# Kernel tuning notes

Hardware: AMD Instinct MI355X
Metric: run time of the kernel (lower is better)

## Reference

```python
import jax, jax.numpy as jnp
import numpy as np

H = W = 32
CROP = int(H * 0.8)  # 25, matches int(H*crop_ratio) in torch
MEAN = jnp.array([0.5071, 0.4867, 0.4408], jnp.float32).reshape(1, 3, 1, 1)
STD = jnp.array([0.2675, 0.2565, 0.2761], jnp.float32).reshape(1, 3, 1, 1)


def _bilinear(img, iy, ix):
    # img [C,H,W]; iy/ix [H,W] float pixel coords (reflected+clamped already)
    y0 = jnp.floor(iy); x0 = jnp.floor(ix)
    wy = iy - y0; wx = ix - x0
    y0i = jnp.clip(y0.astype(jnp.int32), 0, H - 1); y1i = jnp.clip(y0i + 1, 0, H - 1)
    x0i = jnp.clip(x0.astype(jnp.int32), 0, W - 1); x1i = jnp.clip(x0i + 1, 0, W - 1)
    v00 = img[:, y0i, x0i]; v01 = img[:, y0i, x1i]
    v10 = img[:, y1i, x0i]; v11 = img[:, y1i, x1i]
    return v00 * (1 - wy) * (1 - wx) + v01 * (1 - wy) * wx + v10 * wy * (1 - wx) + v11 * wy * wx


def _reflect(c, size):
    # PyTorch grid_sample reflection padding, align_corners=False (reflect about -0.5 / size-0.5)
    lo = -0.5
    span = float(size)
    t = jnp.abs(c - lo)
    extra = jnp.mod(t, span)
    flips = jnp.floor(t / span)
    out = jnp.where(jnp.mod(flips, 2.0) == 0.0, lo + extra, lo + span - extra)
    return jnp.clip(out, 0.0, size - 1.0)


def _crop_resize_one(img, top, left):
    # bilinear resize of img[:, top:top+CROP, left:left+CROP] -> HxW, align_corners=False
    d = (jnp.arange(W, dtype=jnp.float32) + 0.5) * (CROP / W) - 0.5
    d = jnp.maximum(d, 0.0)
    i0 = jnp.floor(d).astype(jnp.int32)
    lam = d - i0
    i1 = jnp.minimum(i0 + 1, CROP - 1)
    r0 = top + i0; r1 = top + i1; c0 = left + i0; c1 = left + i1
    v00 = img[:, r0[:, None], c0[None, :]]
    v01 = img[:, r0[:, None], c1[None, :]]
    v10 = img[:, r1[:, None], c0[None, :]]
    v11 = img[:, r1[:, None], c1[None, :]]
    ly = lam[:, None]; lx = lam[None, :]
    return v00 * (1 - ly) * (1 - lx) + v01 * (1 - ly) * lx + v10 * ly * (1 - lx) + v11 * ly * lx


def _grid_sample_one(img, theta):
    # affine_grid + grid_sample (bilinear, reflection, align_corners=False)
    xs = (2.0 * (jnp.arange(W, dtype=jnp.float32) + 0.5) / W) - 1.0
    ys = (2.0 * (jnp.arange(H, dtype=jnp.float32) + 0.5) / H) - 1.0
    yn, xn = jnp.meshgrid(ys, xs, indexing='ij')
    gx = theta[0, 0] * xn + theta[0, 1] * yn + theta[0, 2]
    gy = theta[1, 0] * xn + theta[1, 1] * yn + theta[1, 2]
    ix = _reflect(((gx + 1.0) * W - 1.0) * 0.5, W)
    iy = _reflect(((gy + 1.0) * H - 1.0) * 0.5, H)
    return _bilinear(img, iy, ix)


def _augment(x, shared_affine, apply_crop):
    B = x.shape[0]
    ks = jax.random.split(jax.random.key(42), 10)
    x = x * STD + MEAN  # de-normalize
    if apply_crop:
        max_off = H - CROP
        top = jax.random.randint(ks[0], (B,), 0, max_off + 1)
        left = jax.random.randint(ks[1], (B,), 0, max_off + 1)
        x = jax.vmap(_crop_resize_one)(x, top, left)
    flip_mask = jax.random.uniform(ks[2], (B,)) < 0.5
    x = jnp.where(flip_mask[:, None, None, None], x[..., ::-1], x)
    # shared affine is provided -> always applied (torch shared_affine branch)
    x = jax.vmap(_grid_sample_one)(x, shared_affine)
    brightness = 1.0 + (jax.random.uniform(ks[3], (B, 1, 1, 1)) - 0.5) * 0.8
    x = x * brightness
    gray = x.mean(axis=1, keepdims=True)
    contrast = 1.0 + (jax.random.uniform(ks[4], (B, 1, 1, 1)) - 0.5) * 0.8
    x = gray + (x - gray) * contrast
    gray = x.mean(axis=1, keepdims=True)
    saturation = 1.0 + (jax.random.uniform(ks[5], (B, 1, 1, 1)) - 0.5) * 0.8
    x = gray + (x - gray) * saturation
    hue_mask = jax.random.uniform(ks[6], (B,)) < 0.5
    x = jnp.where(hue_mask[:, None, None, None], x[:, ::-1], x)  # BGR swap
    gray_mask = jax.random.uniform(ks[7], (B,)) < 0.2
    x = jnp.where(gray_mask[:, None, None, None], x.mean(axis=1, keepdims=True), x)
    blur_mask = jax.random.uniform(ks[8], (B,)) < 0.5
    xp = jnp.pad(x, ((0, 0), (0, 0), (1, 1), (1, 1)), mode='edge')  # replicate pad
    bl = sum(xp[:, :, i:i + H, j:j + W] for i in range(3) for j in range(3)) / 9.0  # 3x3 box blur
    x = jnp.where(blur_mask[:, None, None, None], bl, x)
    solar_mask = jax.random.uniform(ks[9], (B,)) < 0.1
    x = jnp.where(solar_mask[:, None, None, None] & (x > 0.5), 1.0 - x, x)
    x = jnp.clip(x, 0.0, 1.0)
    x = (x - MEAN) / STD  # re-normalize
    return x, flip_mask


def setup_inputs() -> dict:
    key = jax.random.key(0)
    k1, k2 = jax.random.split(key)
    B = 8192
    x = jax.random.normal(k1, (B, 3, H, W), jnp.float32)
    eye = jnp.broadcast_to(jnp.array([[1.0, 0.0, 0.0], [0.0, 1.0, 0.0]], jnp.float32), (B, 2, 3))
    shared_affine = eye + 0.1 * jax.random.normal(k2, (B, 2, 3), jnp.float32)
    return {"x": x, "shared_affine": shared_affine, "apply_crop": 1}


def reference(x, shared_affine, apply_crop):
    out, flip_mask = _augment(x, shared_affine, int(apply_crop))
    # torch returns (x, {'flip': flip_mask, 'affine': affine_theta})
    return out, flip_mask, shared_affine
```

## Files before the change

kernel.cpp:

```cpp
#include <hip/hip_runtime.h>

#define HW 32
#define NPIX 1024
#define IMG 3072
#define IPB 4

typedef float vf4 __attribute__((ext_vector_type(4)));

__device__ __forceinline__ unsigned rotl32(unsigned x, int d) {
    return (x << d) | (x >> (32 - d));
}

struct UPair { unsigned a, b; };

__device__ __forceinline__ UPair threefry2x32(unsigned k0, unsigned k1,
                                              unsigned x0, unsigned x1) {
    unsigned k2 = k0 ^ k1 ^ 0x1BD11BDAu;
    x0 += k0; x1 += k1;
#define RND(r) { x0 += x1; x1 = rotl32(x1, (r)); x1 ^= x0; }
    RND(13) RND(15) RND(26) RND(6)
    x0 += k1; x1 += k2 + 1u;
    RND(17) RND(29) RND(16) RND(24)
    x0 += k2; x1 += k0 + 2u;
    RND(13) RND(15) RND(26) RND(6)
    x0 += k0; x1 += k1 + 3u;
    RND(17) RND(29) RND(16) RND(24)
    x0 += k1; x1 += k2 + 4u;
    RND(13) RND(15) RND(26) RND(6)
    x0 += k2; x1 += k0 + 5u;
#undef RND
    return {x0, x1};
}

__device__ __forceinline__ float bits_to_u01(unsigned bits) {
    return __uint_as_float((bits >> 9) | 0x3f800000u) - 1.0f;
}

__device__ __forceinline__ float reflect32(float c) {
    float t = fabsf(c + 0.5f);
    float flips = floorf(t * 0.03125f);
    float extra = fmaf(flips, -32.0f, t);
    float o = (((int)flips) & 1) ? (31.5f - extra) : (extra - 0.5f);
    return fminf(fmaxf(o, 0.0f), 31.0f);
}

__global__ __launch_bounds__(256) void aug_kernel(
    const float* __restrict__ xin, const float* __restrict__ aff,
    const int* __restrict__ apply_crop, float* __restrict__ out, int B) {
    __shared__ vf4 buf[NPIX];

    const int t = threadIdx.x;
    const int x = t & 31;
    const int yr = t >> 5;
    const int lane = t & 63;
    const bool do_crop = (apply_crop[0] != 0);
    const size_t OUT_IMG = (size_t)B * IMG;
    const int img0 = blockIdx.x * IPB;

    float dxv = fmaxf(fmaf((float)x, 0.78125f, -0.109375f), 0.0f);
    const int q0c = (int)dxv; const float lxc = dxv - (float)q0c;
    const int q1c = min(q0c + 1, 24);
    const float omxc = 1.0f - lxc;
    const float xn = (float)x * 0.0625f - 0.96875f;
    int i0a[4], i1a[4]; float lya[4], yna[4];
#pragma unroll
    for (int i = 0; i < 4; ++i) {
        int yi = yr + 8 * i;
        float dy = fmaxf(fmaf((float)yi, 0.78125f, -0.109375f), 0.0f);
        i0a[i] = (int)dy; lya[i] = dy - (float)i0a[i];
        i1a[i] = min(i0a[i] + 1, 24);
        yna[i] = (float)yi * 0.0625f - 0.96875f;
    }

    float g0[4], g1[4], g2[4];
    {
        const float* src = xin + (size_t)img0 * IMG;
#pragma unroll
        for (int i = 0; i < 4; ++i) {
            int p = t + 256 * i;
            g0[i] = src[p]; g1[i] = src[NPIX + p]; g2[i] = src[2 * NPIX + p];
        }
    }

    for (int k = 0; k < IPB; ++k) {
        const int b = img0 + k;
        if (b >= B) break;

        float fval = 0.0f; int ival = 0;
        if (lane < 10) {
            UPair K = threefry2x32(0u, 42u, 0u, (unsigned)lane);
            if (lane < 2) {
                UPair k2 = threefry2x32(K.a, K.b, 0u, 1u);
                UPair r = threefry2x32(k2.a, k2.b, 0u, (unsigned)b);
                ival = (int)((r.a ^ r.b) & 7u);
            } else {
                UPair r = threefry2x32(K.a, K.b, 0u, (unsigned)b);
                float u = bits_to_u01(r.a ^ r.b);
                if      (lane == 2) ival = (u < 0.5f);
                else if (lane == 3) fval = 1.0f + (u - 0.5f) * 0.8f;
                else if (lane == 4) fval = 1.0f + (u - 0.5f) * 0.8f;
                else if (lane == 5) fval = 1.0f + (u - 0.5f) * 0.8f;
                else if (lane == 6) ival = (u < 0.5f);
                else if (lane == 7) ival = (u < 0.2f);
                else if (lane == 8) ival = (u < 0.5f);
                else                ival = (u < 0.1f);
            }
        }
        const int top  = __shfl(ival, 0), left = __shfl(ival, 1);
        const int flip = __shfl(ival, 2), hue  = __shfl(ival, 6);
        const int gray = __shfl(ival, 7), blur = __shfl(ival, 8);
        const int solar = __shfl(ival, 9);
        const float br   = __shfl(fval, 3);
        const float ctsa = __shfl(fval, 4) * __shfl(fval, 5);
        const float th0 = aff[b * 6 + 0], th1 = aff[b * 6 + 1], th2 = aff[b * 6 + 2];
        const float th3 = aff[b * 6 + 3], th4 = aff[b * 6 + 4], th5 = aff[b * 6 + 5];

#pragma unroll
        for (int i = 0; i < 4; ++i) {
            vf4 v;
            v.x = fmaf(g0[i], 0.2675f, 0.5071f);
            v.y = fmaf(g1[i], 0.2565f, 0.4867f);
            v.z = fmaf(g2[i], 0.2761f, 0.4408f);
            v.w = 0.0f;
            buf[t + 256 * i] = v;
        }

        if (k + 1 < IPB && b + 1 < B) {
            const float* src = xin + (size_t)(b + 1) * IMG;
#pragma unroll
            for (int i = 0; i < 4; ++i) {
                int p = t + 256 * i;
                g0[i] = src[p]; g1[i] = src[NPIX + p]; g2[i] = src[2 * NPIX + p];
            }
        }

        if (t == 0) out[OUT_IMG + b] = flip ? 1.0f : 0.0f;
        if (t < 6)  out[OUT_IMG + (size_t)B + (size_t)b * 6 + t] = aff[b * 6 + t];

        __syncthreads();

        float cx[4], cy[4], cz[4];

        if (do_crop) {
            const int c0 = left + q0c, c1 = left + q1c;
#pragma unroll
            for (int i = 0; i < 4; ++i) {
                int r0 = (top + i0a[i]) << 5, r1 = (top + i1a[i]) << 5;
                float ly = lya[i], omy = 1.0f - ly;
                float w00 = omy * omxc, w01 = omy * lxc;
                float w10 = ly * omxc, w11 = ly * lxc;
                vf4 t00 = buf[r0 + c0], t01 = buf[r0 + c1];
                vf4 t10 = buf[r1 + c0], t11 = buf[r1 + c1];
                cx[i] = fmaf(t00.x, w00, fmaf(t01.x, w01, fmaf(t10.x, w10, t11.x * w11)));
                cy[i] = fmaf(t00.y, w00, fmaf(t01.y, w01, fmaf(t10.y, w10, t11.y * w11)));
                cz[i] = fmaf(t00.z, w00, fmaf(t01.z, w01, fmaf(t10.z, w10, t11.z * w11)));
            }
            __syncthreads();
#pragma unroll
            for (int i = 0; i < 4; ++i) {
                vf4 v; v.x = cx[i]; v.y = cy[i]; v.z = cz[i]; v.w = 0.0f;
                buf[t + 256 * i] = v;
            }
            __syncthreads();
        }

#pragma unroll
        for (int i = 0; i < 4; ++i) {
            float gx = fmaf(th0, xn, fmaf(th1, yna[i], th2));
            float gy = fmaf(th3, xn, fmaf(th4, yna[i], th5));
            float ix = reflect32(fmaf(gx, 16.0f, 15.5f));
            float iy = reflect32(fmaf(gy, 16.0f, 15.5f));
            float fy = floorf(iy), fx = floorf(ix);
            float wy = iy - fy, wx = ix - fx;
            int y0 = (int)fy; int y1 = min(y0 + 1, 31);
            int x0 = (int)fx; int x1 = min(x0 + 1, 31);
            if (flip) { x0 = 31 - x0; x1 = 31 - x1; }
            int r0 = y0 << 5, r1 = y1 << 5;
            float omy = 1.0f - wy, omx = 1.0f - wx;
            float w00 = omy * omx, w01 = omy * wx;
            float w10 = wy * omx, w11 = wy * wx;
            vf4 t00 = buf[r0 + x0], t01 = buf[r0 + x1];
            vf4 t10 = buf[r1 + x0], t11 = buf[r1 + x1];
            float ch0 = fmaf(t00.x, w00, fmaf(t01.x, w01, fmaf(t10.x, w10, t11.x * w11)));
            float ch1 = fmaf(t00.y, w00, fmaf(t01.y, w01, fmaf(t10.y, w10, t11.y * w11)));
            float ch2 = fmaf(t00.z, w00, fmaf(t01.z, w01, fmaf(t10.z, w10, t11.z * w11)));
            ch0 *= br; ch1 *= br; ch2 *= br;
            float g = (ch0 + ch1 + ch2) * (1.0f / 3.0f);
            ch0 = fmaf(ch0 - g, ctsa, g);
            ch1 = fmaf(ch1 - g, ctsa, g);
            ch2 = fmaf(ch2 - g, ctsa, g);
            if (hue) { float tmp = ch0; ch0 = ch2; ch2 = tmp; }
            if (gray) { ch0 = ch1 = ch2 = g; }
            cx[i] = ch0; cy[i] = ch1; cz[i] = ch2;
        }

        if (blur) {
            __syncthreads();
            const int tl = t - 1, tr = t + 1;
            float hx[4], hy[4], hz[4];
#pragma unroll
            for (int i = 0; i < 4; ++i) {
                float v, lf, rt;
                v = cx[i]; lf = __shfl(v, tl); rt = __shfl(v, tr);
                if (x == 0) lf = v;  if (x == 31) rt = v;
                hx[i] = lf + v + rt;
                v = cy[i]; lf = __shfl(v, tl); rt = __shfl(v, tr);
                if (x == 0) lf = v;  if (x == 31) rt = v;
                hy[i] = lf + v + rt;
                v = cz[i]; lf = __shfl(v, tl); rt = __shfl(v, tr);
                if (x == 0) lf = v;  if (x == 31) rt = v;
                hz[i] = lf + v + rt;
            }
#pragma unroll
            for (int i = 0; i < 4; ++i) {
                vf4 v; v.x = hx[i]; v.y = hy[i]; v.z = hz[i]; v.w = 0.0f;
                buf[t + 256 * i] = v;
            }
            __syncthreads();
#pragma unroll
            for (int i = 0; i < 4; ++i) {
                int yi = yr + 8 * i;
                vf4 up = buf[(max(yi - 1, 0) << 5) + x];
                vf4 dn = buf[(min(yi + 1, 31) << 5) + x];
                cx[i] = (up.x + hx[i] + dn.x) * (1.0f / 9.0f);
                cy[i] = (up.y + hy[i] + dn.y) * (1.0f / 9.0f);
                cz[i] = (up.z + hz[i] + dn.z) * (1.0f / 9.0f);
            }
        }

        {
            const float INV0 = 1.0f / 0.2675f, INV1 = 1.0f / 0.2565f, INV2 = 1.0f / 0.2761f;
            float* o = out + (size_t)b * IMG;
#pragma unroll
            for (int i = 0; i < 4; ++i) {
                int p = t + 256 * i;
                float r0v = cx[i], r1v = cy[i], r2v = cz[i];
                if (solar) {
                    if (r0v > 0.5f) r0v = 1.0f - r0v;
                    if (r1v > 0.5f) r1v = 1.0f - r1v;
                    if (r2v > 0.5f) r2v = 1.0f - r2v;
                }
                r0v = fminf(fmaxf(r0v, 0.0f), 1.0f);
                r1v = fminf(fmaxf(r1v, 0.0f), 1.0f);
                r2v = fminf(fmaxf(r2v, 0.0f), 1.0f);
                __builtin_nontemporal_store((r0v - 0.5071f) * INV0, o + p);
                __builtin_nontemporal_store((r1v - 0.4867f) * INV1, o + NPIX + p);
                __builtin_nontemporal_store((r2v - 0.4408f) * INV2, o + 2 * NPIX + p);
            }
        }

        if (k + 1 < IPB && b + 1 < B) __syncthreads();
    }
}

extern "C" void kernel_launch(void* const* d_in, const int* in_sizes, int n_in,
                              void* d_out, int out_size, void* d_ws, size_t ws_size,
                              hipStream_t stream) {
    const float* x = (const float*)d_in[0];
    const float* aff = (const float*)d_in[1];
    const int* ac = (const int*)d_in[2];
    float* out = (float*)d_out;
    int B = in_sizes[0] / IMG;
    int grid = (B + IPB - 1) / IPB;
    aug_kernel<<<dim3(grid), dim3(256), 0, stream>>>(x, aff, ac, out, B);
}
```

Measured before the change: 206.1 us.

## Precompute per-image RNG params in LDS, halve images per block, raise occupancy

After: 209.9 us. No clear change (+1.9%).

```diff
diff --git a/kernel.cpp b/kernel.cpp
--- a/kernel.cpp
+++ b/kernel.cpp
@@ -3,7 +3,7 @@
 #define HW 32
 #define NPIX 1024
 #define IMG 3072
-#define IPB 4
+#define IPB 2
 
 typedef float vf4 __attribute__((ext_vector_type(4)));
 
@@ -44,76 +44,77 @@
     return fminf(fmaxf(o, 0.0f), 31.0f);
 }
 
-__global__ __launch_bounds__(256) void aug_kernel(
+__device__ __forceinline__ float rfl_f(float v) {
+    return __uint_as_float(__builtin_amdgcn_readfirstlane(__float_as_uint(v)));
+}
+__device__ __forceinline__ int rfl_i(int v) {
+    return __builtin_amdgcn_readfirstlane(v);
+}
+
+__global__ __launch_bounds__(256, 8) void aug_kernel(
     const float* __restrict__ xin, const float* __restrict__ aff,
     const int* __restrict__ apply_crop, float* __restrict__ out, int B) {
     __shared__ vf4 buf[NPIX];
+    __shared__ float s_pf[2][9];
+    __shared__ int   s_pi[2][7];
 
     const int t = threadIdx.x;
     const int x = t & 31;
     const int yr = t >> 5;
-    const int lane = t & 63;
     const bool do_crop = (apply_crop[0] != 0);
     const size_t OUT_IMG = (size_t)B * IMG;
     const int img0 = blockIdx.x * IPB;
+
+    float g0[4], g1[4], g2[4];
+    {
+        const float* src = xin + (size_t)img0 * IMG;
+#pragma unroll
+        for (int i = 0; i < 4; ++i) {
+            int p = t + 256 * i;
+            g0[i] = src[p]; g1[i] = src[NPIX + p]; g2[i] = src[2 * NPIX + p];
+        }
+    }
+
+    if (t < 12) {
+        int slot = t / 6, j = t - slot * 6;
+        int bb = img0 + slot;
+        if (bb < B) s_pf[slot][j] = aff[(size_t)bb * 6 + j];
+    }
+    if (t >= 32 && t < 52) {
+        int u10 = t - 32;
+        int slot = u10 / 10, kk = u10 - slot * 10;
+        int bb = img0 + slot;
+        if (bb < B) {
+            UPair K = threefry2x32(0u, 42u, 0u, (unsigned)kk);
+            if (kk < 2) {
+                UPair k2 = threefry2x32(K.a, K.b, 0u, 1u);
+                UPair r = threefry2x32(k2.a, k2.b, 0u, (unsigned)bb);
+                s_pi[slot][kk] = (int)((r.a ^ r.b) & 7u);
+            } else {
+                UPair r = threefry2x32(K.a, K.b, 0u, (unsigned)bb);
+                float u = bits_to_u01(r.a ^ r.b);
+                if      (kk == 2) s_pi[slot][2] = (u < 0.5f);
+                else if (kk == 3) s_pf[slot][6] = 1.0f + (u - 0.5f) * 0.8f;
+                else if (kk == 4) s_pf[slot][7] = 1.0f + (u - 0.5f) * 0.8f;
+                else if (kk == 5) s_pf[slot][8] = 1.0f + (u - 0.5f) * 0.8f;
+                else if (kk == 6) s_pi[slot][3] = (u < 0.5f);
+                else if (kk == 7) s_pi[slot][4] = (u < 0.2f);
+                else if (kk == 8) s_pi[slot][5] = (u < 0.5f);
+                else              s_pi[slot][6] = (u < 0.1f);
+            }
+        }
+    }
 
     float dxv = fmaxf(fmaf((float)x, 0.78125f, -0.109375f), 0.0f);
     const int q0c = (int)dxv; const float lxc = dxv - (float)q0c;
     const int q1c = min(q0c + 1, 24);
     const float omxc = 1.0f - lxc;
     const float xn = (float)x * 0.0625f - 0.96875f;
-    int i0a[4], i1a[4]; float lya[4], yna[4];
-#pragma unroll
-    for (int i = 0; i < 4; ++i) {
-        int yi = yr + 8 * i;
-        float dy = fmaxf(fmaf((float)yi, 0.78125f, -0.109375f), 0.0f);
-        i0a[i] = (int)dy; lya[i] = dy - (float)i0a[i];
-        i1a[i] = min(i0a[i] + 1, 24);
-        yna[i] = (float)yi * 0.0625f - 0.96875f;
-    }
-
-    float g0[4], g1[4], g2[4];
-    {
-        const float* src = xin + (size_t)img0 * IMG;
-#pragma unroll
-        for (int i = 0; i < 4; ++i) {
-            int p = t + 256 * i;
-            g0[i] = src[p]; g1[i] = src[NPIX + p]; g2[i] = src[2 * NPIX + p];
-        }
-    }
-
+
+#pragma unroll
     for (int k = 0; k < IPB; ++k) {
         const int b = img0 + k;
         if (b >= B) break;
-
-        float fval = 0.0f; int ival = 0;
-        if (lane < 10) {
-            UPair K = threefry2x32(0u, 42u, 0u, (unsigned)lane);
-            if (lane < 2) {
-                UPair k2 = threefry2x32(K.a, K.b, 0u, 1u);
-                UPair r = threefry2x32(k2.a, k2.b, 0u, (unsigned)b);
-                ival = (int)((r.a ^ r.b) & 7u);
-            } else {
-                UPair r = threefry2x32(K.a, K.b, 0u, (unsigned)b);
-                float u = bits_to_u01(r.a ^ r.b);
-                if      (lane == 2) ival = (u < 0.5f);
-                else if (lane == 3) fval = 1.0f + (u - 0.5f) * 0.8f;
-                else if (lane == 4) fval = 1.0f + (u - 0.5f) * 0.8f;
-                else if (lane == 5) fval = 1.0f + (u - 0.5f) * 0.8f;
-                else if (lane == 6) ival = (u < 0.5f);
-                else if (lane == 7) ival = (u < 0.2f);
-                else if (lane == 8) ival = (u < 0.5f);
-                else                ival = (u < 0.1f);
-            }
-        }
-        const int top  = __shfl(ival, 0), left = __shfl(ival, 1);
-        const int flip = __shfl(ival, 2), hue  = __shfl(ival, 6);
-        const int gray = __shfl(ival, 7), blur = __shfl(ival, 8);
-        const int solar = __shfl(ival, 9);
-        const float br   = __shfl(fval, 3);
-        const float ctsa = __shfl(fval, 4) * __shfl(fval, 5);
-        const float th0 = aff[b * 6 + 0], th1 = aff[b * 6 + 1], th2 = aff[b * 6 + 2];
-        const float th3 = aff[b * 6 + 3], th4 = aff[b * 6 + 4], th5 = aff[b * 6 + 5];
 
 #pragma unroll
         for (int i = 0; i < 4; ++i) {
@@ -134,10 +135,20 @@
             }
         }
 
+        __syncthreads();
+
+        const int top  = rfl_i(s_pi[k][0]), left = rfl_i(s_pi[k][1]);
+        const int flip = rfl_i(s_pi[k][2]), hue  = rfl_i(s_pi[k][3]);
+        const int gray = rfl_i(s_pi[k][4]), blur = rfl_i(s_pi[k][5]);
+        const int solar = rfl_i(s_pi[k][6]);
+        const float br   = rfl_f(s_pf[k][6]);
+        const float ctsa = rfl_f(s_pf[k][7]) * rfl_f(s_pf[k][8]);
+        const float th0 = rfl_f(s_pf[k][0]), th1 = rfl_f(s_pf[k][1]);
+        const float th2 = rfl_f(s_pf[k][2]), th3 = rfl_f(s_pf[k][3]);
+        const float th4 = rfl_f(s_pf[k][4]), th5 = rfl_f(s_pf[k][5]);
+
         if (t == 0) out[OUT_IMG + b] = flip ? 1.0f : 0.0f;
-        if (t < 6)  out[OUT_IMG + (size_t)B + (size_t)b * 6 + t] = aff[b * 6 + t];
-
-        __syncthreads();
+        if (t < 6)  out[OUT_IMG + (size_t)B + (size_t)b * 6 + t] = s_pf[k][t];
 
         float cx[4], cy[4], cz[4];
 
@@ -145,8 +156,11 @@
             const int c0 = left + q0c, c1 = left + q1c;
 #pragma unroll
             for (int i = 0; i < 4; ++i) {
-                int r0 = (top + i0a[i]) << 5, r1 = (top + i1a[i]) << 5;
-                float ly = lya[i], omy = 1.0f - ly;
+                int yi = yr + 8 * i;
+                float dy = fmaxf(fmaf((float)yi, 0.78125f, -0.109375f), 0.0f);
+                int i0 = (int)dy; float ly = dy - (float)i0; int i1 = min(i0 + 1, 24);
+                int r0 = (top + i0) << 5, r1 = (top + i1) << 5;
+                float omy = 1.0f - ly;
                 float w00 = omy * omxc, w01 = omy * lxc;
                 float w10 = ly * omxc, w11 = ly * lxc;
                 vf4 t00 = buf[r0 + c0], t01 = buf[r0 + c1];
@@ -166,8 +180,10 @@
 
 #pragma unroll
         for (int i = 0; i < 4; ++i) {
-            float gx = fmaf(th0, xn, fmaf(th1, yna[i], th2));
-            float gy = fmaf(th3, xn, fmaf(th4, yna[i], th5));
+            int yi = yr + 8 * i;
+            float yn = (float)yi * 0.0625f - 0.96875f;
+            float gx = fmaf(th0, xn, fmaf(th1, yn, th2));
+            float gy = fmaf(th3, xn, fmaf(th4, yn, th5));
             float ix = reflect32(fmaf(gx, 16.0f, 15.5f));
             float iy = reflect32(fmaf(gy, 16.0f, 15.5f));
             float fy = floorf(iy), fx = floorf(ix);
```
